# Kernel optimization log

Hardware: AMD Instinct MI355X
Metric: run time of the kernel (lower is better)

## Reference

```python
import jax, jax.numpy as jnp
import numpy as np

C = 64
D = C // 8  # query/key channels
B, H, W = 4, 64, 64


def setup_inputs() -> dict:
    key = jax.random.key(0)
    ks = jax.random.split(key, 8)
    x = jax.random.normal(ks[0], (B, C, H, W), dtype=jnp.float32)
    # 1x1 conv params (kernel squeezed to [out_ch, in_ch])
    sq = 1.0 / np.sqrt(C)
    Wq = jax.random.uniform(ks[1], (D, C), jnp.float32, -sq, sq)
    bq = jax.random.uniform(ks[2], (D,), jnp.float32, -sq, sq)
    Wk = jax.random.uniform(ks[3], (D, C), jnp.float32, -sq, sq)
    bk = jax.random.uniform(ks[4], (D,), jnp.float32, -sq, sq)
    Wv = jax.random.uniform(ks[5], (C, C), jnp.float32, -sq, sq)
    bv = jax.random.uniform(ks[6], (C,), jnp.float32, -sq, sq)
    # gamma is zero-initialized in the module; use a nonzero value so the
    # attention path actually contributes to the output.
    gamma = jax.random.normal(ks[7], (1,), dtype=jnp.float32)
    return {"x": x, "Wq": Wq, "bq": bq, "Wk": Wk, "bk": bk, "Wv": Wv, "bv": bv, "gamma": gamma}


def reference(x, Wq, bq, Wk, bk, Wv, bv, gamma):
    b, c, h, w = x.shape
    n = h * w
    xf = x.reshape(b, c, n)                                   # [B,C,N]
    q = jnp.einsum('dc,bcn->bdn', Wq, xf) + bq[None, :, None]  # [B,D,N]
    k = jnp.einsum('dc,bcn->bdn', Wk, xf) + bk[None, :, None]  # [B,D,N]
    v = jnp.einsum('ec,bcn->ben', Wv, xf) + bv[None, :, None]  # [B,C,N]
    energy = jnp.einsum('bdn,bdm->bnm', q, k)                  # [B,N,N] = Q^T K
    attn = jax.nn.softmax(energy, axis=-1)                     # softmax over keys m
    # out[b,c,n] = sum_m v[b,c,m] * attn[b,n,m]  (V @ attention^T in torch)
    out = jnp.einsum('bcm,bnm->bcn', v, attn).reshape(b, c, h, w)
    return gamma[0] * out + x
```

## Files before the change

kernel.cpp:

```cpp
#include <hip/hip_runtime.h>
#include <hip/hip_bf16.h>
#include <math.h>

#define BB 4
#define CC 64
#define DD 8
#define NN 4096
#define KS 16
#define KPS (NN / KS)
#define VSTR 260
#define KSTR 12
#define LOG2E 1.44269504088896340736f

typedef __attribute__((ext_vector_type(4))) short short4v;
typedef __attribute__((ext_vector_type(4))) unsigned short ushort4v;
typedef __attribute__((ext_vector_type(8))) unsigned short ushort8;
typedef __attribute__((ext_vector_type(16))) float f32x16;

#if defined(__HIP_DEVICE_COMPILE__)
  #if __has_builtin(__builtin_amdgcn_mfma_f32_32x32x8bf16_1k)
    #define MFMA32x8(A, B, C) __builtin_amdgcn_mfma_f32_32x32x8bf16_1k(A, B, C, 0, 0, 0)
  #elif __has_builtin(__builtin_amdgcn_mfma_f32_32x32x8_bf16)
    #define MFMA32x8(A, B, C) __builtin_amdgcn_mfma_f32_32x32x8_bf16(A, B, C, 0, 0, 0)
  #else
    #error "no 32x32x8 bf16 MFMA builtin in device pass"
  #endif
  #if __has_builtin(__builtin_amdgcn_exp2f)
    #define EXP2(x) __builtin_amdgcn_exp2f(x)
  #else
    #define EXP2(x) exp2f(x)
  #endif
#else
  static __device__ __host__ inline f32x16 MFMA32x8(short4v, short4v, f32x16 c) { return c; }
  #define EXP2(x) exp2f(x)
#endif

static __device__ inline short4v pack4(float a, float b, float c, float d) {
    union { short4v s; __hip_bfloat162 h[2]; } u;
    u.h[0] = __float22bfloat162_rn(make_float2(a, b));
    u.h[1] = __float22bfloat162_rn(make_float2(c, d));
    return u.s;
}
static __device__ inline unsigned packu(float lo, float hi) {
    union { __hip_bfloat162 h; unsigned u; } t;
    t.h = __float22bfloat162_rn(make_float2(lo, hi));
    return t.u;
}

__global__ __launch_bounds__(256) void qkv_kernel(
    const float* __restrict__ x,  const float* __restrict__ Wq, const float* __restrict__ bq,
    const float* __restrict__ Wk, const float* __restrict__ bk,
    const float* __restrict__ Wv, const float* __restrict__ bv,
    unsigned short* __restrict__ qb, unsigned short* __restrict__ kb,
    unsigned short* __restrict__ vT)
{
    __shared__ unsigned short LQ[128 * 8];
    __shared__ unsigned short LK[128 * 8];

    int tid = threadIdx.x;
    int wave = tid >> 6, lane = tid & 63;
    int l32 = lane & 31, h2 = lane >> 5;

    int blk = blockIdx.x;
    int b = blk & (BB - 1);
    int r2 = blk >> 2;
    int rt = r2 % 3;
    int ng = r2 / 3;
    int n0 = ng * 128 + wave * 32;

    short4v af[8];
    #pragma unroll
    for (int s = 0; s < 8; ++s) {
        float4 w4;
        if (rt < 2) {
            w4 = *(const float4*)(Wv + (size_t)(rt * 32 + l32) * CC + s * 8 + 4 * h2);
        } else if (l32 < 8) {
            w4 = *(const float4*)(Wq + (size_t)l32 * CC + s * 8 + 4 * h2);
        } else if (l32 < 16) {
            w4 = *(const float4*)(Wk + (size_t)(l32 - 8) * CC + s * 8 + 4 * h2);
        } else {
            w4 = make_float4(0.f, 0.f, 0.f, 0.f);
        }
        af[s] = pack4(w4.x, w4.y, w4.z, w4.w);
    }

    const float* xb = x + (size_t)b * CC * NN + n0 + l32;
    short4v bf[8];
    #pragma unroll
    for (int s = 0; s < 8; ++s) {
        int c0 = s * 8 + 4 * h2;
        float x0 = xb[(size_t)(c0 + 0) * NN];
        float x1 = xb[(size_t)(c0 + 1) * NN];
        float x2 = xb[(size_t)(c0 + 2) * NN];
        float x3 = xb[(size_t)(c0 + 3) * NN];
        bf[s] = pack4(x0, x1, x2, x3);
    }

    f32x16 acc;
    #pragma unroll
    for (int r = 0; r < 16; ++r) acc[r] = 0.f;
    #pragma unroll
    for (int s = 0; s < 8; ++s)
        acc = MFMA32x8(af[s], bf[s], acc);

    if (rt < 2) {
        #pragma unroll
        for (int r = 0; r < 16; ++r) {
            int row = rt * 32 + (r & 3) + 8 * (r >> 2) + 4 * h2;
            float val = acc[r] + bv[row];
            __hip_bfloat16 hv = __float2bfloat16(val);
            vT[((size_t)b * CC + row) * NN + n0 + l32] = *(unsigned short*)&hv;
        }
    } else {
        short4v qp = pack4((acc[0] + bq[0 + 4 * h2]) * LOG2E,
                           (acc[1] + bq[1 + 4 * h2]) * LOG2E,
                           (acc[2] + bq[2 + 4 * h2]) * LOG2E,
                           (acc[3] + bq[3 + 4 * h2]) * LOG2E);
        short4v kp = pack4(acc[4] + bk[0 + 4 * h2],
                           acc[5] + bk[1 + 4 * h2],
                           acc[6] + bk[2 + 4 * h2],
                           acc[7] + bk[3 + 4 * h2]);
        int nl = wave * 32 + l32;
        *(short4v*)(LQ + (size_t)nl * 8 + 4 * h2) = qp;
        *(short4v*)(LK + (size_t)nl * 8 + 4 * h2) = kp;
        __syncthreads();
        if (tid < 128) {
            ushort8 row = *(const ushort8*)(LQ + (size_t)tid * 8);
            *(ushort8*)(qb + ((size_t)b * NN + ng * 128 + tid) * 8) = row;
        } else {
            int t = tid - 128;
            ushort8 row = *(const ushort8*)(LK + (size_t)t * 8);
            *(ushort8*)(kb + ((size_t)b * NN + ng * 128 + t) * 8) = row;
        }
    }
}

__global__ __launch_bounds__(512, 6) void flash_kernel(
    const unsigned short* __restrict__ qb, const unsigned short* __restrict__ kb,
    const unsigned short* __restrict__ vT, unsigned* __restrict__ accb,
    float* __restrict__ sbuf)
{
    __shared__ unsigned short VS[64 * VSTR];
    __shared__ unsigned short KL[256 * KSTR];
    int tid = threadIdx.x;
    int wave = tid >> 6, lane = tid & 63;
    int l32 = lane & 31, h2 = lane >> 5;

    int blk = blockIdx.x;
    int b = blk & (BB - 1);
    int rest = blk >> 2;
    int split = rest & (KS - 1);
    int qchunk = rest >> 4;
    int n0 = qchunk * 256 + wave * 32;

    short4v qf = *(const short4v*)(qb + ((size_t)b * NN + n0 + l32) * DD + h2 * 4);

    const unsigned short* kbb = kb + (size_t)b * NN * DD;
    const unsigned short* vbb = vT + (size_t)b * CC * NN;
    int m0 = split * KPS;

    int ch = tid >> 3, ks0 = (tid & 7) * 32;
    {
        const unsigned short* vg = vbb + (size_t)ch * NN + m0 + ks0;
        ushort8 v0 = *(const ushort8*)(vg);
        ushort8 v1 = *(const ushort8*)(vg + 8);
        ushort8 v2 = *(const ushort8*)(vg + 16);
        ushort8 v3 = *(const ushort8*)(vg + 24);
        ushort8 kA = {0,0,0,0,0,0,0,0};
        if (tid < 256) kA = *(const ushort8*)(kbb + (size_t)(m0 + tid) * DD);

        unsigned short* vp = VS + (size_t)ch * VSTR + ks0;
        *(ushort4v*)(vp)      = *(ushort4v*)&v0;
        *(ushort4v*)(vp + 4)  = *((ushort4v*)&v0 + 1);
        *(ushort4v*)(vp + 8)  = *(ushort4v*)&v1;
        *(ushort4v*)(vp + 12) = *((ushort4v*)&v1 + 1);
        *(ushort4v*)(vp + 16) = *(ushort4v*)&v2;
        *(ushort4v*)(vp + 20) = *((ushort4v*)&v2 + 1);
        *(ushort4v*)(vp + 24) = *(ushort4v*)&v3;
        *(ushort4v*)(vp + 28) = *((ushort4v*)&v3 + 1);
        if (tid < 256) {
            unsigned short* p = KL + (size_t)tid * KSTR;
            *(ushort4v*)(p)     = *(ushort4v*)&kA;
            *(ushort4v*)(p + 4) = *((ushort4v*)&kA + 1);
        }
    }
    __syncthreads();

    f32x16 o0, o1, zz;
    #pragma unroll
    for (int r = 0; r < 16; ++r) { o0[r] = 0.f; o1[r] = 0.f; zz[r] = 0.f; }
    float s0 = 0.f, s1 = 0.f, s2 = 0.f, s3 = 0.f;

    #pragma unroll
    for (int s = 0; s < 8; ++s) {
        short4v kf = *(const short4v*)(KL + (size_t)(s * 32 + l32) * KSTR + h2 * 4);
        f32x16 st = MFMA32x8(kf, qf, zz);
        float w[16];
        #pragma unroll
        for (int r = 0; r < 16; ++r) w[r] = EXP2(st[r]);
        s0 += (w[0] + w[1]) + (w[2] + w[3]);
        s1 += (w[4] + w[5]) + (w[6] + w[7]);
        s2 += (w[8] + w[9]) + (w[10] + w[11]);
        s3 += (w[12] + w[13]) + (w[14] + w[15]);

        union { short4v s; __hip_bfloat162 h[2]; } u[4];
        #pragma unroll
        for (int g = 0; g < 4; ++g) {
            u[g].h[0] = __float22bfloat162_rn(make_float2(w[4 * g],     w[4 * g + 1]));
            u[g].h[1] = __float22bfloat162_rn(make_float2(w[4 * g + 2], w[4 * g + 3]));
        }
        #pragma unroll
        for (int g = 0; g < 4; ++g) {
            int gg = s * 4 + g;
            short4v vf0 = *(const short4v*)(VS + (size_t)(l32)      * VSTR + gg * 8 + h2 * 4);
            short4v vf1 = *(const short4v*)(VS + (size_t)(32 + l32) * VSTR + gg * 8 + h2 * 4);
            o0 = MFMA32x8(u[g].s, vf0, o0);
            o1 = MFMA32x8(u[g].s, vf1, o1);
        }
    }

    unsigned* au = accb + (((size_t)((b * KS + split) * 128 + qchunk * 8 + wave)) << 10);
    #pragma unroll
    for (int r = 0; r < 16; ++r)
        au[r * 64 + lane] = packu(o0[r], o1[r]);

    float ssum = (s0 + s1) + (s2 + s3);
    ssum += __shfl_xor(ssum, 32);
    if (lane < 32)
        sbuf[(size_t)(b * KS + split) * NN + n0 + l32] = ssum;
}

__global__ __launch_bounds__(256) void norm_kernel(
    const unsigned* __restrict__ accb, const float* __restrict__ sbuf,
    const float* __restrict__ x, const float* __restrict__ gamma,
    float* __restrict__ out)
{
    __shared__ float tile[16 * 65];
    __shared__ float stl[16];
    int blk = blockIdx.x;
    int b = blk >> 8;
    int h = blk & 255;
    int g32 = h >> 1;
    int qhalf = h & 1;
    int n0 = g32 * 32 + qhalf * 16;
    int tid = threadIdx.x;

    if (tid < 16) {
        float st = 0.f;
        #pragma unroll
        for (int sp = 0; sp < KS; ++sp)
            st += sbuf[(size_t)(b * KS + sp) * NN + n0 + tid];
        stl[tid] = 1.0f / st;
    }

    int spoff = tid >> 7;
    int u = tid & 127;
    int rl = u >> 4;
    int lane0 = (u & 15) * 4;

    float alo[4], ahi[4];
    #pragma unroll
    for (int e = 0; e < 4; ++e) { alo[e] = 0.f; ahi[e] = 0.f; }
    #pragma unroll
    for (int p = 0; p < 8; ++p) {
        int sp = p * 2 + spoff;
        const unsigned* base = accb + (((size_t)((b * KS + sp) * 128 + g32)) << 10)
                             + qhalf * 512;
        uint4 v = *(const uint4*)(base + u * 4);
        unsigned wv[4] = {v.x, v.y, v.z, v.w};
        #pragma unroll
        for (int e = 0; e < 4; ++e) {
            alo[e] += __uint_as_float(wv[e] << 16);
            ahi[e] += __uint_as_float(wv[e] & 0xFFFF0000u);
        }
    }

    #pragma unroll
    for (int e = 0; e < 4; ++e) {
        int lane = lane0 + e;
        int h2 = lane >> 5, l32 = lane & 31;
        int ql = (rl & 3) + 8 * ((rl >> 2) & 1) + 4 * h2;
        if (tid < 128) {
            tile[ql * 65 + l32]      = alo[e];
            tile[ql * 65 + 32 + l32] = ahi[e];
        }
    }
    __syncthreads();
    #pragma unroll
    for (int e = 0; e < 4; ++e) {
        int lane = lane0 + e;
        int h2 = lane >> 5, l32 = lane & 31;
        int ql = (rl & 3) + 8 * ((rl >> 2) & 1) + 4 * h2;
        if (tid >= 128) {
            tile[ql * 65 + l32]      += alo[e];
            tile[ql * 65 + 32 + l32] += ahi[e];
        }
    }
    __syncthreads();

    float gm = gamma[0];
    #pragma unroll
    for (int p2 = 0; p2 < 4; ++p2) {
        int idx = p2 * 256 + tid;
        int c = idx >> 4, ql = idx & 15;
        size_t xi = ((size_t)b * CC + c) * NN + n0 + ql;
        out[xi] = gm * tile[ql * 65 + c] * stl[ql] + x[xi];
    }
}

extern "C" void kernel_launch(void* const* d_in, const int* in_sizes, int n_in,
                              void* d_out, int out_size, void* d_ws, size_t ws_size,
                              hipStream_t stream)
{
    const float* x     = (const float*)d_in[0];
    const float* Wq    = (const float*)d_in[1];
    const float* bq    = (const float*)d_in[2];
    const float* Wk    = (const float*)d_in[3];
    const float* bk    = (const float*)d_in[4];
    const float* Wv    = (const float*)d_in[5];
    const float* bv    = (const float*)d_in[6];
    const float* gamma = (const float*)d_in[7];
    float* out = (float*)d_out;

    float* ws = (float*)d_ws;
    size_t off = 0;
    unsigned short* qb = (unsigned short*)(ws + off); off += (size_t)BB * NN * DD / 2 + 64;
    unsigned short* kb = (unsigned short*)(ws + off); off += (size_t)BB * NN * DD / 2 + 64;
    unsigned short* vT = (unsigned short*)(ws + off); off += (size_t)BB * CC * NN / 2 + 64;
    unsigned* accb = (unsigned*)(ws + off); off += (size_t)BB * KS * NN * CC / 2;
    float* sbuf = ws + off; off += (size_t)BB * KS * NN;

    qkv_kernel<<<BB * 3 * 32, 256, 0, stream>>>(x, Wq, bq, Wk, bk, Wv, bv, qb, kb, vT);
    flash_kernel<<<BB * 16 * KS, 512, 0, stream>>>(qb, kb, vT, accb, sbuf);
    norm_kernel<<<BB * 256, 256, 0, stream>>>(accb, sbuf, x, gamma, out);
}
```

Before: 101.5 us.

## Halve key splits, double-buffer V/K tiles via direct global-to-LDS loads

The key dimension is now split into 8 chunks instead of 16, so each block processes two 256-key stages. The V tile is loaded straight into LDS with global_load_lds and an XOR-swizzled layout that replaces the padded stride. The second stage's loads are issued before the first stage computes, so they overlap. Fewer splits also shrink the partial accumulator traffic in the normalize kernel, in exchange for half as many blocks, more LDS per block and a lower occupancy hint.

```diff
diff --git a/kernel.cpp b/kernel.cpp
--- a/kernel.cpp
+++ b/kernel.cpp
@@ -6,9 +6,8 @@
 #define CC 64
 #define DD 8
 #define NN 4096
-#define KS 16
+#define KS 8
 #define KPS (NN / KS)
-#define VSTR 260
 #define KSTR 12
 #define LOG2E 1.44269504088896340736f
 
@@ -34,6 +33,18 @@
   static __device__ __host__ inline f32x16 MFMA32x8(short4v, short4v, f32x16 c) { return c; }
   #define EXP2(x) exp2f(x)
 #endif
+
+static __device__ __forceinline__ void gll16(const unsigned short* g,
+                                             unsigned short* l, int lane) {
+#if defined(__HIP_DEVICE_COMPILE__) && __has_builtin(__builtin_amdgcn_global_load_lds)
+    __builtin_amdgcn_global_load_lds(
+        (const __attribute__((address_space(1))) unsigned int*)g,
+        (__attribute__((address_space(3))) unsigned int*)l, 16, 0, 0);
+    (void)lane;
+#else
+    *(ushort8*)((char*)l + (size_t)lane * 16) = *(const ushort8*)g;
+#endif
+}
 
 static __device__ inline short4v pack4(float a, float b, float c, float d) {
     union { short4v s; __hip_bfloat162 h[2]; } u;
@@ -135,65 +146,17 @@
     }
 }
 
-__global__ __launch_bounds__(512, 6) void flash_kernel(
-    const unsigned short* __restrict__ qb, const unsigned short* __restrict__ kb,
-    const unsigned short* __restrict__ vT, unsigned* __restrict__ accb,
-    float* __restrict__ sbuf)
-{
-    __shared__ unsigned short VS[64 * VSTR];
-    __shared__ unsigned short KL[256 * KSTR];
-    int tid = threadIdx.x;
-    int wave = tid >> 6, lane = tid & 63;
-    int l32 = lane & 31, h2 = lane >> 5;
-
-    int blk = blockIdx.x;
-    int b = blk & (BB - 1);
-    int rest = blk >> 2;
-    int split = rest & (KS - 1);
-    int qchunk = rest >> 4;
-    int n0 = qchunk * 256 + wave * 32;
-
-    short4v qf = *(const short4v*)(qb + ((size_t)b * NN + n0 + l32) * DD + h2 * 4);
-
-    const unsigned short* kbb = kb + (size_t)b * NN * DD;
-    const unsigned short* vbb = vT + (size_t)b * CC * NN;
-    int m0 = split * KPS;
-
-    int ch = tid >> 3, ks0 = (tid & 7) * 32;
-    {
-        const unsigned short* vg = vbb + (size_t)ch * NN + m0 + ks0;
-        ushort8 v0 = *(const ushort8*)(vg);
-        ushort8 v1 = *(const ushort8*)(vg + 8);
-        ushort8 v2 = *(const ushort8*)(vg + 16);
-        ushort8 v3 = *(const ushort8*)(vg + 24);
-        ushort8 kA = {0,0,0,0,0,0,0,0};
-        if (tid < 256) kA = *(const ushort8*)(kbb + (size_t)(m0 + tid) * DD);
-
-        unsigned short* vp = VS + (size_t)ch * VSTR + ks0;
-        *(ushort4v*)(vp)      = *(ushort4v*)&v0;
-        *(ushort4v*)(vp + 4)  = *((ushort4v*)&v0 + 1);
-        *(ushort4v*)(vp + 8)  = *(ushort4v*)&v1;
-        *(ushort4v*)(vp + 12) = *((ushort4v*)&v1 + 1);
-        *(ushort4v*)(vp + 16) = *(ushort4v*)&v2;
-        *(ushort4v*)(vp + 20) = *((ushort4v*)&v2 + 1);
-        *(ushort4v*)(vp + 24) = *(ushort4v*)&v3;
-        *(ushort4v*)(vp + 28) = *((ushort4v*)&v3 + 1);
-        if (tid < 256) {
-            unsigned short* p = KL + (size_t)tid * KSTR;
-            *(ushort4v*)(p)     = *(ushort4v*)&kA;
-            *(ushort4v*)(p + 4) = *((ushort4v*)&kA + 1);
-        }
-    }
-    __syncthreads();
-
-    f32x16 o0, o1, zz;
-    #pragma unroll
-    for (int r = 0; r < 16; ++r) { o0[r] = 0.f; o1[r] = 0.f; zz[r] = 0.f; }
-    float s0 = 0.f, s1 = 0.f, s2 = 0.f, s3 = 0.f;
-
+static __device__ __forceinline__ void compute_stage(
+    const unsigned short* VSst, const unsigned short* KLst,
+    short4v qf, int l32, int h2,
+    f32x16& o0, f32x16& o1, float& s0, float& s1, float& s2, float& s3)
+{
+    f32x16 zz;
+    #pragma unroll
+    for (int r = 0; r < 16; ++r) zz[r] = 0.f;
     #pragma unroll
     for (int s = 0; s < 8; ++s) {
-        short4v kf = *(const short4v*)(KL + (size_t)(s * 32 + l32) * KSTR + h2 * 4);
+        short4v kf = *(const short4v*)(KLst + (size_t)(s * 32 + l32) * KSTR + h2 * 4);
         f32x16 st = MFMA32x8(kf, qf, zz);
         float w[16];
         #pragma unroll
@@ -211,13 +174,78 @@
         }
         #pragma unroll
         for (int g = 0; g < 4; ++g) {
-            int gg = s * 4 + g;
-            short4v vf0 = *(const short4v*)(VS + (size_t)(l32)      * VSTR + gg * 8 + h2 * 4);
-            short4v vf1 = *(const short4v*)(VS + (size_t)(32 + l32) * VSTR + gg * 8 + h2 * 4);
+            int go = (((s * 4 + g) ^ (l32 & 7)) * 8) + h2 * 4;
+            short4v vf0 = *(const short4v*)(VSst + (size_t)(l32)      * 256 + go);
+            short4v vf1 = *(const short4v*)(VSst + (size_t)(32 + l32) * 256 + go);
             o0 = MFMA32x8(u[g].s, vf0, o0);
             o1 = MFMA32x8(u[g].s, vf1, o1);
         }
     }
+}
+
+__global__ __launch_bounds__(512, 4) void flash_kernel(
+    const unsigned short* __restrict__ qb, const unsigned short* __restrict__ kb,
+    const unsigned short* __restrict__ vT, unsigned* __restrict__ accb,
+    float* __restrict__ sbuf)
+{
+    __shared__ unsigned short VS[2][64 * 256];
+    __shared__ unsigned short KL[2][256 * KSTR];
+    int tid = threadIdx.x;
+    int wave = tid >> 6, lane = tid & 63;
+    int l32 = lane & 31, h2 = lane >> 5;
+
+    int blk = blockIdx.x;
+    int b = blk & (BB - 1);
+    int rest = blk >> 2;
+    int split = rest & (KS - 1);
+    int qchunk = rest >> 3;
+    int n0 = qchunk * 256 + wave * 32;
+
+    short4v qf = *(const short4v*)(qb + ((size_t)b * NN + n0 + l32) * DD + h2 * 4);
+
+    const unsigned short* kbb = kb + (size_t)b * NN * DD;
+    const unsigned short* vbb = vT + (size_t)b * CC * NN;
+    int m0 = split * KPS;
+
+    int chv[4], offv[4];
+    #pragma unroll
+    for (int i = 0; i < 4; ++i) {
+        chv[i] = 8 * wave + 2 * i + h2;
+        offv[i] = chv[i] * NN + 8 * (l32 ^ (chv[i] & 7));
+    }
+
+    #pragma unroll
+    for (int i = 0; i < 4; ++i)
+        gll16(vbb + offv[i] + m0, &VS[0][(size_t)(wave * 4 + i) * 512], lane);
+    if (tid < 256) {
+        ushort8 kA = *(const ushort8*)(kbb + (size_t)(m0 + tid) * DD);
+        unsigned short* p = &KL[0][(size_t)tid * KSTR];
+        *(ushort4v*)(p)     = *(ushort4v*)&kA;
+        *(ushort4v*)(p + 4) = *((ushort4v*)&kA + 1);
+    }
+    __syncthreads();
+
+    ushort8 kB = {0,0,0,0,0,0,0,0};
+    if (tid < 256) kB = *(const ushort8*)(kbb + (size_t)(m0 + 256 + tid) * DD);
+    #pragma unroll
+    for (int i = 0; i < 4; ++i)
+        gll16(vbb + offv[i] + m0 + 256, &VS[1][(size_t)(wave * 4 + i) * 512], lane);
+
+    f32x16 o0, o1;
+    #pragma unroll
+    for (int r = 0; r < 16; ++r) { o0[r] = 0.f; o1[r] = 0.f; }
+    float s0 = 0.f, s1 = 0.f, s2 = 0.f, s3 = 0.f;
+
+    compute_stage(VS[0], KL[0], qf, l32, h2, o0, o1, s0, s1, s2, s3);
+
+    if (tid < 256) {
+        unsigned short* p = &KL[1][(size_t)tid * KSTR];
+        *(ushort4v*)(p)     = *(ushort4v*)&kB;
+        *(ushort4v*)(p + 4) = *((ushort4v*)&kB + 1);
+    }
+    __syncthreads();
+
+    compute_stage(VS[1], KL[1], qf, l32, h2, o0, o1, s0, s1, s2, s3);
 
     unsigned* au = accb + (((size_t)((b * KS + split) * 128 + qchunk * 8 + wave)) << 10);
     #pragma unroll
@@ -262,7 +290,7 @@
     #pragma unroll
     for (int e = 0; e < 4; ++e) { alo[e] = 0.f; ahi[e] = 0.f; }
     #pragma unroll
-    for (int p = 0; p < 8; ++p) {
+    for (int p = 0; p < KS / 2; ++p) {
         int sp = p * 2 + spoff;
         const unsigned* base = accb + (((size_t)((b * KS + sp) * 128 + g32)) << 10)
                              + qhalf * 512;
```

After: 121.4 us. 19.7% more time.
